# Kernel tuning notes

Measured on AMD Instinct MI355X. Metric: run time of the kernel, lower is better.

The kernel has to match this reference:

```python
import jax, jax.numpy as jnp
import numpy as np
from jax import lax

SCALES = (1, 4, 16, 64)
EPS = 1e-5
B, S, D, H, R, FF = 4, 1024, 512, 8, 4, 2048
C = D // len(SCALES)  # channels per temporal scale


def _ln(x, g, b):
    mu = jnp.mean(x, -1, keepdims=True)
    var = jnp.mean(jnp.square(x - mu), -1, keepdims=True)
    return (x - mu) * lax.rsqrt(var + EPS) * g + b


def _interp_linear(y, L_out):
    # y: [B, C, L_in]; torch F.interpolate(mode='linear', align_corners=False)
    L_in = y.shape[-1]
    if L_in == L_out:
        return y
    pos = (jnp.arange(L_out, dtype=jnp.float32) + 0.5) * (L_in / L_out) - 0.5
    pos = jnp.clip(pos, 0.0, L_in - 1)
    lo = jnp.floor(pos).astype(jnp.int32)
    hi = jnp.minimum(lo + 1, L_in - 1)
    w = (pos - lo.astype(jnp.float32))
    return y[..., lo] * (1.0 - w) + y[..., hi] * w


def _conv1d(x, w, b, stride):
    # x: [B, Cin, L], w: [Cout, Cin, K]
    y = lax.conv_general_dilated(x, w, window_strides=(stride,), padding='VALID',
                                 dimension_numbers=('NCH', 'OIH', 'NCH'))
    return y + b[None, :, None]


def setup_inputs() -> dict:
    key = jax.random.key(0)
    ks = jax.random.split(key, 40)
    n = lambda k, shp, s=0.02: jax.random.normal(k, shp, jnp.float32) * s
    inp = {}
    inp['x'] = jax.random.normal(ks[0], (B, S, D), jnp.float32)
    inp['resource_mask'] = jax.random.randint(ks[1], (B, S), 0, R, jnp.int32)
    inp['attention_mask'] = jnp.ones((B, S), jnp.int32)
    inp['wq'] = n(ks[2], (D, D)); inp['bq'] = jnp.zeros((D,), jnp.float32)
    inp['wk'] = n(ks[3], (D, D)); inp['bk'] = jnp.zeros((D,), jnp.float32)
    inp['wv'] = n(ks[4], (D, D)); inp['bv'] = jnp.zeros((D,), jnp.float32)
    inp['wo'] = n(ks[5], (D, D)); inp['bo'] = jnp.zeros((D,), jnp.float32)
    inp['rbias'] = jax.random.normal(ks[6], (H, R, R), jnp.float32)
    for i, sc in enumerate(SCALES):
        inp[f'cw{i}'] = n(ks[7 + i], (C, D, sc))
        inp[f'cb{i}'] = jnp.zeros((C,), jnp.float32)
    inp['fw'] = n(ks[12], (D, D)); inp['fb'] = jnp.zeros((D,), jnp.float32)
    inp['ltg'] = jnp.ones((D,), jnp.float32); inp['ltb'] = jnp.zeros((D,), jnp.float32)
    inp['n1g'] = jnp.ones((D,), jnp.float32); inp['n1b'] = jnp.zeros((D,), jnp.float32)
    inp['n2g'] = jnp.ones((D,), jnp.float32); inp['n2b'] = jnp.zeros((D,), jnp.float32)
    inp['fw1'] = n(ks[13], (FF, D)); inp['fb1'] = jnp.zeros((FF,), jnp.float32)
    inp['fw2'] = n(ks[14], (D, FF)); inp['fb2'] = jnp.zeros((D,), jnp.float32)
    inp['n3g'] = jnp.ones((D,), jnp.float32); inp['n3b'] = jnp.zeros((D,), jnp.float32)
    return inp


def reference(x, resource_mask, attention_mask, wq, bq, wk, bk, wv, bv, wo, bo, rbias,
              cw0, cb0, cw1, cb1, cw2, cb2, cw3, cb3, fw, fb, ltg, ltb,
              n1g, n1b, n2g, n2b, fw1, fb1, fw2, fb2, n3g, n3b):
    b_, s_, d_ = x.shape
    dk = d_ // H
    # --- ResourceAwareAttention (dropout = identity in eval) ---
    q = (x @ wq.T + bq).reshape(b_, s_, H, dk).transpose(0, 2, 1, 3)
    k = (x @ wk.T + bk).reshape(b_, s_, H, dk).transpose(0, 2, 1, 3)
    v = (x @ wv.T + bv).reshape(b_, s_, H, dk).transpose(0, 2, 1, 3)
    scores = jnp.einsum('bhid,bhjd->bhij', q, k) / jnp.sqrt(jnp.float32(dk))
    # vectorized resource-bias gather: bias[b,h,i,j] = rbias[h, rm[b,i], rm[b,j]]
    idx_h = jnp.arange(H)[None, :, None, None]
    idx_i = resource_mask[:, None, :, None]
    idx_j = resource_mask[:, None, None, :]
    scores = scores + rbias[idx_h, idx_i, idx_j]
    scores = jnp.where(attention_mask[:, None, None, :] == 0, -1e9, scores)
    attn = jax.nn.softmax(scores, axis=-1)
    o = jnp.einsum('bhij,bhjd->bhid', attn, v).transpose(0, 2, 1, 3).reshape(b_, s_, d_)
    attn_out = o @ wo.T + bo
    x = _ln(x + attn_out, n1g, n1b)
    # --- MultiScaleTemporalEncoder ---
    xc = x.transpose(0, 2, 1)  # [B, D, S]
    convs = ((cw0, cb0), (cw1, cb1), (cw2, cb2), (cw3, cb3))
    outs = []
    for sc, (w, bb) in zip(SCALES, convs):
        y = _conv1d(xc, w, bb, sc)  # [B, C, S/sc]
        outs.append(_interp_linear(y, s_))
    ms = jnp.concatenate(outs, axis=1).transpose(0, 2, 1)  # [B, S, D]
    fused = ms @ fw.T + fb
    temporal = _ln(x + fused, ltg, ltb)
    x = _ln(x + temporal, n2g, n2b)
    # --- FFN ---
    ff = jax.nn.relu(x @ fw1.T + fb1) @ fw2.T + fb2
    return _ln(x + ff, n3g, n3b)
```

## Files before the change

kernel.cpp:

```cpp
#include <hip/hip_runtime.h>
#include <math.h>

constexpr int B_ = 4, S_ = 1024, D_ = 512, H_ = 8, FF_ = 2048;
constexpr int DK_ = 64;
constexpr int C_ = 128;
constexpr int QKVLD = 1536;

typedef __bf16 bf16x8 __attribute__((ext_vector_type(8)));
typedef __bf16 bf16x4 __attribute__((ext_vector_type(4)));
typedef short short4v __attribute__((ext_vector_type(4)));
typedef float floatx4 __attribute__((ext_vector_type(4)));

__device__ __forceinline__ void g2l16(const __bf16* g, __bf16* l) {
  __builtin_amdgcn_global_load_lds(
      (__attribute__((address_space(1))) void*)(unsigned long long)g,
      (__attribute__((address_space(3))) void*)(unsigned int)(unsigned long long)l,
      16, 0, 0);
}

__device__ __forceinline__ int xcd_swz(int lin, int nwg) {
  return (lin & 7) * (nwg >> 3) + (lin >> 3);
}

template <bool OUTBF16, bool RELU, bool WRITEVT>
__global__ __launch_bounds__(256, 2) void mgemm(
    const __bf16* __restrict__ A, const __bf16* __restrict__ W,
    const float* __restrict__ bias, void* __restrict__ Yv,
    int M, int N, int K, int ldY, __bf16* __restrict__ VT) {
  __shared__ __bf16 As[2][128 * 64];
  __shared__ __bf16 Bs[2][128 * 64];
  const int tid = threadIdx.x;
  const int wave = tid >> 6, lane = tid & 63;
  const int nwg = gridDim.x * gridDim.y;
  const int lin = blockIdx.y * gridDim.x + blockIdx.x;
  const int swz = xcd_swz(lin, nwg);
  const int bm = (swz / gridDim.x) * 128, bn = (swz % gridDim.x) * 128;

  const int rsub = lane >> 3;
  const int gch = ((lane & 7) ^ rsub) * 8;
  const __bf16* gA = A + (size_t)(bm + wave * 32 + rsub) * K + gch;
  const __bf16* gB = W + (size_t)(bn + wave * 32 + rsub) * K + gch;

  const int mrow = lane & 15, g4 = lane >> 4;
  const int rsw = mrow & 7;
  const int wm = (wave & 1) * 64, wn = (wave >> 1) * 64;

  floatx4 acc[4][4];
#pragma unroll
  for (int mi = 0; mi < 4; mi++)
#pragma unroll
    for (int ni = 0; ni < 4; ni++) acc[mi][ni] = (floatx4){0.f, 0.f, 0.f, 0.f};

  const int nk = K >> 6;
  auto stage = [&](int buf, int kt) {
    const __bf16* ga = gA + (size_t)kt * 64;
    const __bf16* gb = gB + (size_t)kt * 64;
    __bf16* la = &As[buf][wave * 32 * 64];
    __bf16* lb = &Bs[buf][wave * 32 * 64];
#pragma unroll
    for (int i = 0; i < 4; i++) {
      g2l16(ga + (size_t)(i * 8) * K, la + i * 8 * 64);
      g2l16(gb + (size_t)(i * 8) * K, lb + i * 8 * 64);
    }
  };

  stage(0, 0);
  int cur = 0;
  for (int kk = 0; kk < nk; kk++) {
    __syncthreads();
    if (kk + 1 < nk) stage(cur ^ 1, kk + 1);
    const __bf16* Ab = As[cur];
    const __bf16* Bb = Bs[cur];
#pragma unroll
    for (int c = 0; c < 2; c++) {
      const int pc = (((c * 4 + g4) ^ rsw)) * 8;
      bf16x8 af[4], bfr[4];
#pragma unroll
      for (int mi = 0; mi < 4; mi++)
        af[mi] = *(const bf16x8*)(Ab + (wm + mi * 16 + mrow) * 64 + pc);
#pragma unroll
      for (int ni = 0; ni < 4; ni++)
        bfr[ni] = *(const bf16x8*)(Bb + (wn + ni * 16 + mrow) * 64 + pc);
#pragma unroll
      for (int mi = 0; mi < 4; mi++)
#pragma unroll
        for (int ni = 0; ni < 4; ni++)
          acc[mi][ni] = __builtin_amdgcn_mfma_f32_16x16x32_bf16(af[mi], bfr[ni], acc[mi][ni], 0, 0, 0);
    }
    cur ^= 1;
  }

  const int cc = lane & 15;
  const int r0 = (lane >> 4) * 4;
  float bv[4];
#pragma unroll
  for (int ni = 0; ni < 4; ni++) bv[ni] = bias[bn + wn + ni * 16 + cc];
#pragma unroll
  for (int mi = 0; mi < 4; mi++) {
#pragma unroll
    for (int ni = 0; ni < 4; ni++) {
      const int col = bn + wn + ni * 16 + cc;
      if (WRITEVT && col >= 1024) {
        const int h = (col - 1024) >> 6, d = (col - 1024) & 63;
        const int rowb = bm + wm + mi * 16 + r0;
        const int b = rowb >> 10, s = rowb & 1023;
        union { __bf16 hh[4]; unsigned long long u; } w;
#pragma unroll
        for (int i = 0; i < 4; i++) w.hh[i] = (__bf16)(acc[mi][ni][i] + bv[ni]);
        *(unsigned long long*)(VT + (size_t)(b * 8 + h) * 65536 + (size_t)d * 1024 + s) = w.u;
      } else {
#pragma unroll
        for (int i = 0; i < 4; i++) {
          float v = acc[mi][ni][i] + bv[ni];
          if (RELU) v = fmaxf(v, 0.f);
          const size_t row = bm + wm + mi * 16 + r0 + i;
          if (OUTBF16)
            ((__bf16*)Yv)[row * ldY + col] = (__bf16)v;
          else
            ((float*)Yv)[row * ldY + col] = v;
        }
      }
    }
  }
}

template <bool OUTBF16, bool RELU>
__global__ __launch_bounds__(256, 2) void mgemm64(
    const __bf16* __restrict__ A, const __bf16* __restrict__ W,
    const float* __restrict__ bias, void* __restrict__ Yv,
    int M, int N, int K, int ldY) {
  __shared__ __bf16 As[2][64 * 64];
  __shared__ __bf16 Bs[2][64 * 64];
  const int tid = threadIdx.x;
  const int wave = tid >> 6, lane = tid & 63;
  const int nwg = gridDim.x * gridDim.y;
  const int lin = blockIdx.y * gridDim.x + blockIdx.x;
  const int swz = xcd_swz(lin, nwg);
  const int bm = (swz / gridDim.x) * 64, bn = (swz % gridDim.x) * 64;

  const int rsub = lane >> 3;
  const int gch = ((lane & 7) ^ rsub) * 8;
  const __bf16* gA = A + (size_t)(bm + wave * 16 + rsub) * K + gch;
  const __bf16* gB = W + (size_t)(bn + wave * 16 + rsub) * K + gch;

  const int mrow = lane & 15, g4 = lane >> 4;
  const int rsw = mrow & 7;
  const int wm = (wave & 1) * 32, wn = (wave >> 1) * 32;

  floatx4 acc[2][2];
#pragma unroll
  for (int mi = 0; mi < 2; mi++)
#pragma unroll
    for (int ni = 0; ni < 2; ni++) acc[mi][ni] = (floatx4){0.f, 0.f, 0.f, 0.f};

  const int nk = K >> 6;
  auto stage = [&](int buf, int kt) {
    const __bf16* ga = gA + (size_t)kt * 64;
    const __bf16* gb = gB + (size_t)kt * 64;
    __bf16* la = &As[buf][wave * 16 * 64];
    __bf16* lb = &Bs[buf][wave * 16 * 64];
#pragma unroll
    for (int i = 0; i < 2; i++) {
      g2l16(ga + (size_t)(i * 8) * K, la + i * 8 * 64);
      g2l16(gb + (size_t)(i * 8) * K, lb + i * 8 * 64);
    }
  };

  stage(0, 0);
  int cur = 0;
  for (int kk = 0; kk < nk; kk++) {
    __syncthreads();
    if (kk + 1 < nk) stage(cur ^ 1, kk + 1);
    const __bf16* Ab = As[cur];
    const __bf16* Bb = Bs[cur];
#pragma unroll
    for (int c = 0; c < 2; c++) {
      const int pc = (((c * 4 + g4) ^ rsw)) * 8;
      bf16x8 af[2], bfr[2];
#pragma unroll
      for (int mi = 0; mi < 2; mi++)
        af[mi] = *(const bf16x8*)(Ab + (wm + mi * 16 + mrow) * 64 + pc);
#pragma unroll
      for (int ni = 0; ni < 2; ni++)
        bfr[ni] = *(const bf16x8*)(Bb + (wn + ni * 16 + mrow) * 64 + pc);
#pragma unroll
      for (int mi = 0; mi < 2; mi++)
#pragma unroll
        for (int ni = 0; ni < 2; ni++)
          acc[mi][ni] = __builtin_amdgcn_mfma_f32_16x16x32_bf16(af[mi], bfr[ni], acc[mi][ni], 0, 0, 0);
    }
    cur ^= 1;
  }

  const int cc = lane & 15;
  const int r0 = (lane >> 4) * 4;
  float bv[2];
#pragma unroll
  for (int ni = 0; ni < 2; ni++) bv[ni] = bias[bn + wn + ni * 16 + cc];
#pragma unroll
  for (int mi = 0; mi < 2; mi++) {
#pragma unroll
    for (int ni = 0; ni < 2; ni++) {
      const int col = bn + wn + ni * 16 + cc;
#pragma unroll
      for (int i = 0; i < 4; i++) {
        float v = acc[mi][ni][i] + bv[ni];
        if (RELU) v = fmaxf(v, 0.f);
        const size_t row = bm + wm + mi * 16 + r0 + i;
        if (OUTBF16)
          ((__bf16*)Yv)[row * ldY + col] = (__bf16)v;
        else
          ((float*)Yv)[row * ldY + col] = v;
      }
    }
  }
}

__global__ __launch_bounds__(256, 2) void cgemm3(
    const __bf16* __restrict__ A, const __bf16* __restrict__ w4,
    const __bf16* __restrict__ w16, const __bf16* __restrict__ w64,
    const __bf16* __restrict__ w1, const float* __restrict__ cb0,
    float* __restrict__ y1, float* __restrict__ y2, float* __restrict__ y3,
    __bf16* __restrict__ msb) {
  int id = blockIdx.x;
  const __bf16* W;
  float* yseg = nullptr;
  int M, K, bm, k0s;
  bool direct = false;
  if (id < 64) {
    W = w4; yseg = y1; M = 1024; K = 2048;
    bm = (id & 15) * 64; k0s = id >> 4;
  } else if (id < 128) {
    id -= 64;
    W = w16; yseg = y2; M = 256; K = 8192;
    bm = (id & 3) * 64; k0s = id >> 2;
  } else if (id < 192) {
    id -= 128;
    W = w64; yseg = y3; M = 64; K = 32768;
    bm = 0; k0s = id;
  } else {
    id -= 192;
    W = w1; M = 4096; K = 512;
    bm = id * 64; k0s = 0; direct = true;
  }
  const int k0 = k0s * 512;

  __shared__ __bf16 As[2][64 * 32];
  __shared__ __bf16 Bs[2][128 * 32];
  const int tid = threadIdx.x;
  const int wave = tid >> 6, lane = tid & 63;

  const int rs2 = lane >> 2;
  const int ssw2 = (rs2 & 3) ^ ((rs2 >> 2) & 3);
  const int gc2 = ((lane & 3) ^ ssw2) * 8;
  const __bf16* gA = A + (size_t)(bm + wave * 16 + rs2) * K + k0 + gc2;
  const __bf16* gB0 = W + (size_t)(wave * 16 + rs2) * K + k0 + gc2;
  const __bf16* gB1 = W + (size_t)(64 + wave * 16 + rs2) * K + k0 + gc2;

  const int mrow = lane & 15, g4 = lane >> 4;
  const int fsw = (lane & 3) ^ ((lane >> 2) & 3);
  const int fc = (g4 ^ fsw) & 3;

  floatx4 acc[8];
#pragma unroll
  for (int nj = 0; nj < 8; nj++) acc[nj] = (floatx4){0.f, 0.f, 0.f, 0.f};

  auto stage = [&](int buf, int kt) {
    const size_t ko = (size_t)kt * 32;
    g2l16(gA + ko, &As[buf][wave * 16 * 32]);
    g2l16(gB0 + ko, &Bs[buf][wave * 16 * 32]);
    g2l16(gB1 + ko, &Bs[buf][(64 + wave * 16) * 32]);
  };

  stage(0, 0);
  int cur = 0;
  for (int kk = 0; kk < 16; kk++) {
    __syncthreads();
    if (kk + 1 < 16) stage(cur ^ 1, kk + 1);
    bf16x8 af = *(const bf16x8*)(As[cur] + (wave * 16 + mrow) * 32 + fc * 8);
#pragma unroll
    for (int nj = 0; nj < 8; nj++) {
      bf16x8 bfv = *(const bf16x8*)(Bs[cur] + (nj * 16 + mrow) * 32 + fc * 8);
      acc[nj] = __builtin_amdgcn_mfma_f32_16x16x32_bf16(af, bfv, acc[nj], 0, 0, 0);
    }
    cur ^= 1;
  }

  const int cc = lane & 15;
  const int r0 = (lane >> 4) * 4;
  if (direct) {
#pragma unroll
    for (int nj = 0; nj < 8; nj++) {
      const float bb = cb0[nj * 16 + cc];
#pragma unroll
      for (int i = 0; i < 4; i++)
        msb[(size_t)(bm + wave * 16 + r0 + i) * 512 + nj * 16 + cc] =
            (__bf16)(acc[nj][i] + bb);
    }
  } else {
#pragma unroll
    for (int nj = 0; nj < 8; nj++)
#pragma unroll
      for (int i = 0; i < 4; i++)
        atomicAdd(&yseg[(size_t)(bm + wave * 16 + r0 + i) * 128 + nj * 16 + cc],
                  acc[nj][i]);
  }
}

__global__ __launch_bounds__(256) void prep(
    const float* __restrict__ cw1, const float* __restrict__ cw2,
    const float* __restrict__ cw3, __bf16* __restrict__ wt4,
    __bf16* __restrict__ wt16, __bf16* __restrict__ wt64,
    const float* __restrict__ s0, const float* __restrict__ s1,
    const float* __restrict__ s2, const float* __restrict__ s3,
    const float* __restrict__ s4, const float* __restrict__ s5,
    const float* __restrict__ s6, const float* __restrict__ s7,
    const float* __restrict__ s8,
    __bf16* __restrict__ d0, __bf16* __restrict__ d1, __bf16* __restrict__ d2,
    __bf16* __restrict__ d3, __bf16* __restrict__ d4, __bf16* __restrict__ d5,
    __bf16* __restrict__ d6, __bf16* __restrict__ d7, __bf16* __restrict__ d8,
    const float* __restrict__ bq, const float* __restrict__ bk,
    const float* __restrict__ bv, float* __restrict__ bqkv,
    const float* __restrict__ cb1, const float* __restrict__ cb2,
    const float* __restrict__ cb3, float* __restrict__ yall) {
  __shared__ float Ts[4608];
  const int tid = threadIdx.x;
  if (blockIdx.x < 1408) {
    int id = blockIdx.x;
    const float* cw;
    __bf16* wt;
    int lg, c, d0i, TD, L;
    if (id < 128) {
      cw = cw1; wt = wt4; lg = 2; c = id; d0i = 0; TD = 512; L = 2048;
    } else if (id < 384) {
      id -= 128;
      cw = cw2; wt = wt16; lg = 4; c = id >> 1; d0i = (id & 1) * 256; TD = 256; L = 4096;
    } else {
      id -= 384;
      cw = cw3; wt = wt64; lg = 6; c = id >> 3; d0i = (id & 7) * 64; TD = 64; L = 4096;
    }
    const int sc = 1 << lg;
    const int KD = 512 << lg;
    const float* src = cw + (size_t)c * KD + (size_t)d0i * sc;

    for (int f = tid * 4; f < L; f += 1024) {
      const float4 v = *(const float4*)(src + f);
      const float vv[4] = {v.x, v.y, v.z, v.w};
#pragma unroll
      for (int j = 0; j < 4; j++) {
        const int idx = f + j;
        const int dl = idx >> lg, k = idx & (sc - 1);
        Ts[dl * (sc + 1) + k] = vv[j];
      }
    }
    __syncthreads();

    for (int w = tid * 8; w < L; w += 2048) {
      const int kpos = w / TD;
      const int dl0 = w - kpos * TD;
      union { __bf16 hh[8]; bf16x8 v; } u;
#pragma unroll
      for (int j = 0; j < 8; j++)
        u.hh[j] = (__bf16)Ts[(dl0 + j) * (sc + 1) + kpos];
      *(bf16x8*)(wt + (size_t)c * KD + kpos * 512 + d0i + dl0) = u.v;
    }
    return;
  }

  const int qd = (blockIdx.x - 1408) * 256 + tid;
  if (qd < 384) {
    const int i = qd * 4;
    const float* s;
    int off;
    if (i < 512) { s = bq; off = 0; }
    else if (i < 1024) { s = bk; off = 512; }
    else { s = bv; off = 1024; }
    *(float4*)(bqkv + i) = *(const float4*)(s + i - off);
  }
  if (qd < 172032) {
    float bb;
    if (qd < 131072) bb = cb1[qd & 127];
    else if (qd < 163840) bb = cb2[qd & 127];
    else bb = cb3[qd & 127];
    yall[qd] = bb;
  }
  if (qd >= 1392640) return;
  const float* src;
  __bf16* dst;
  int base;
  if (qd < 524288) { src = s0; dst = d0; base = 0; }
  else if (qd < 589824) { src = s1; dst = d1; base = 524288; }
  else if (qd < 655360) { src = s2; dst = d2; base = 589824; }
  else if (qd < 720896) { src = s3; dst = d3; base = 655360; }
  else if (qd < 786432) { src = s4; dst = d4; base = 720896; }
  else if (qd < 851968) { src = s5; dst = d5; base = 786432; }
  else if (qd < 868352) { src = s6; dst = d6; base = 851968; }
  else if (qd < 1130496) { src = s7; dst = d7; base = 868352; }
  else { src = s8; dst = d8; base = 1130496; }
  const int local = qd - base;
  float4 v = *(const float4*)(src + (size_t)local * 4);
  union { __bf16 h[4]; unsigned long long u; } t;
  t.h[0] = (__bf16)v.x; t.h[1] = (__bf16)v.y;
  t.h[2] = (__bf16)v.z; t.h[3] = (__bf16)v.w;
  *(unsigned long long*)(dst + (size_t)local * 4) = t.u;
}

__global__ __launch_bounds__(256) void fattn(
    const __bf16* __restrict__ QKV, const __bf16* __restrict__ VT,
    const float* __restrict__ rbias, const int* __restrict__ rm,
    const int* __restrict__ amask, __bf16* __restrict__ O) {
  __shared__ __bf16 Ks[64 * 72];
  __shared__ __bf16 Vs[64 * 72];
  __shared__ float T[4 * 1032];

  const int tid = threadIdx.x, wave = tid >> 6, lane = tid & 63;
  const int nwg = gridDim.x * gridDim.y;
  const int lin = blockIdx.y * gridDim.x + blockIdx.x;
  const int swz = xcd_swz(lin, nwg);
  const int qb = swz % gridDim.x;
  const int bh = swz / gridDim.x;
  const int b = bh >> 3, h = bh & 7;
  const int q0 = qb * 64;
  const int cc = lane & 15, quad = lane >> 4;

  for (int j = tid; j < 1024; j += 256) {
    const int rv = rm[b * S_ + j];
    const float mk = amask[b * S_ + j] ? 1.f : 0.f;
#pragma unroll
    for (int ri = 0; ri < 4; ri++)
      T[ri * 1032 + j] = __expf(rbias[h * 16 + ri * 4 + rv]) * mk;
  }

  const int qrow = q0 + wave * 16;
  const int rmi = rm[b * S_ + qrow + cc];
  const float* Trow = T + rmi * 1032;

  const __bf16* Qr = QKV + (size_t)(b * S_ + qrow + cc) * QKVLD + h * 64;
  const bf16x8 qb0 = *(const bf16x8*)(Qr + quad * 8);
  const bf16x8 qb1 = *(const bf16x8*)(Qr + 32 + quad * 8);

  floatx4 of[4];
#pragma unroll
  for (int dc = 0; dc < 4; dc++) of[dc] = (floatx4){0.f, 0.f, 0.f, 0.f};
  float mold = -1e30f, l = 0.f;

  const __bf16* Kbase = QKV + (size_t)(b * S_) * QKVLD + 512 + h * 64;
  const __bf16* Vtbase = VT + (size_t)bh * 65536;
  const int srow = tid >> 2, sch = tid & 3;

  for (int jt = 0; jt < 16; jt++) {
    const int j0 = jt * 64;
    __syncthreads();
    {
      const __bf16* kg = Kbase + (size_t)(j0 + srow) * QKVLD;
      *(bf16x8*)(Ks + srow * 72 + sch * 8) = *(const bf16x8*)(kg + sch * 8);
      *(bf16x8*)(Ks + srow * 72 + 32 + sch * 8) = *(const bf16x8*)(kg + 32 + sch * 8);
      const __bf16* vg = Vtbase + (size_t)srow * 1024 + j0;
      *(bf16x8*)(Vs + srow * 72 + sch * 8) = *(const bf16x8*)(vg + sch * 8);
      *(bf16x8*)(Vs + srow * 72 + 32 + sch * 8) = *(const bf16x8*)(vg + 32 + sch * 8);
    }
    __syncthreads();

    floatx4 st[4];
    __builtin_amdgcn_s_setprio(1);
#pragma unroll
    for (int js = 0; js < 4; js++) {
      const bf16x8 ka0 = *(const bf16x8*)(Ks + (js * 16 + cc) * 72 + quad * 8);
      const bf16x8 ka1 = *(const bf16x8*)(Ks + (js * 16 + cc) * 72 + 32 + quad * 8);
      floatx4 s = (floatx4){0.f, 0.f, 0.f, 0.f};
      s = __builtin_amdgcn_mfma_f32_16x16x32_bf16(ka0, qb0, s, 0, 0, 0);
      s = __builtin_amdgcn_mfma_f32_16x16x32_bf16(ka1, qb1, s, 0, 0, 0);
      st[js] = s;
    }
    __builtin_amdgcn_s_setprio(0);

    float mxr = st[0][0];
#pragma unroll
    for (int js = 0; js < 4; js++)
#pragma unroll
      for (int i = 0; i < 4; i++) mxr = fmaxf(mxr, st[js][i]);
    mxr = fmaxf(mxr, __shfl_xor(mxr, 16));
    mxr = fmaxf(mxr, __shfl_xor(mxr, 32));
    const float mnew = fmaxf(mold, mxr * 0.125f);
    const float alpha = __expf(mold - mnew);
    mold = mnew;

    float rsum = 0.f;
    short4v pk[4];
#pragma unroll
    for (int js = 0; js < 4; js++) {
      const floatx4 Tv = *(const floatx4*)(Trow + j0 + js * 16 + quad * 4);
      union { __bf16 hh[4]; short4v s4; } u;
#pragma unroll
      for (int i = 0; i < 4; i++) {
        const float p = __expf(fmaf(st[js][i], 0.125f, -mnew)) * Tv[i];
        rsum += p;
        u.hh[i] = (__bf16)p;
      }
      pk[js] = u.s4;
    }
    rsum += __shfl_xor(rsum, 16);
    rsum += __shfl_xor(rsum, 32);
    l = l * alpha + rsum;

#pragma unroll
    for (int dc = 0; dc < 4; dc++)
#pragma unroll
      for (int i = 0; i < 4; i++) of[dc][i] *= alpha;

    __builtin_amdgcn_s_setprio(1);
#pragma unroll
    for (int dc = 0; dc < 4; dc++) {
#pragma unroll
      for (int js = 0; js < 4; js++) {
        union { bf16x4 v; short4v s4; } va;
        va.v = *(const bf16x4*)(Vs + (dc * 16 + cc) * 72 + js * 16 + quad * 4);
        of[dc] = __builtin_amdgcn_mfma_f32_16x16x16bf16_1k(va.s4, pk[js], of[dc], 0, 0, 0);
      }
    }
    __builtin_amdgcn_s_setprio(0);
  }

  const float invl = 1.f / l;
  __bf16* po = O + (size_t)(b * S_ + qrow + cc) * D_ + h * 64;
#pragma unroll
  for (int dc = 0; dc < 4; dc++) {
    union { __bf16 hh[4]; unsigned long long u; } w;
#pragma unroll
    for (int i = 0; i < 4; i++) w.hh[i] = (__bf16)(of[dc][i] * invl);
    *(unsigned long long*)(po + dc * 16 + quad * 4) = w.u;
  }
}

__global__ __launch_bounds__(256) void add_ln_kernel(
    const float* __restrict__ xa, const float* __restrict__ xb,
    const float* __restrict__ g, const float* __restrict__ be,
    float* __restrict__ out, __bf16* __restrict__ outb) {
  const int row = (blockIdx.x * 256 + threadIdx.x) >> 6;
  const int lane = threadIdx.x & 63;
  const float* pa = xa + (size_t)row * D_;
  const float* pb = xb + (size_t)row * D_;
  float v[8];
  float sum = 0.f;
#pragma unroll
  for (int i = 0; i < 8; i++) {
    int dd = lane + 64 * i;
    v[i] = pa[dd] + pb[dd];
    sum += v[i];
  }
#pragma unroll
  for (int off = 32; off; off >>= 1) sum += __shfl_xor(sum, off);
  const float mu = sum * (1.f / D_);
  float vs = 0.f;
#pragma unroll
  for (int i = 0; i < 8; i++) { float t = v[i] - mu; vs += t * t; }
#pragma unroll
  for (int off = 32; off; off >>= 1) vs += __shfl_xor(vs, off);
  const float inv = rsqrtf(vs * (1.f / D_) + 1e-5f);
  float* po = out + (size_t)row * D_;
#pragma unroll
  for (int i = 0; i < 8; i++) {
    int dd = lane + 64 * i;
    float o = (v[i] - mu) * inv * g[dd] + be[dd];
    po[dd] = o;
    if (outb) outb[(size_t)row * D_ + dd] = (__bf16)o;
  }
}

__global__ __launch_bounds__(256) void ln_chain_kernel(
    const float* __restrict__ x1, const float* __restrict__ fused,
    const float* __restrict__ ltg, const float* __restrict__ ltb,
    const float* __restrict__ n2g, const float* __restrict__ n2b,
    float* __restrict__ out, __bf16* __restrict__ outb) {
  const int row = (blockIdx.x * 256 + threadIdx.x) >> 6;
  const int lane = threadIdx.x & 63;
  const float* p1 = x1 + (size_t)row * D_;
  const float* pf = fused + (size_t)row * D_;
  float xv[8], u[8];
  float sum = 0.f;
#pragma unroll
  for (int i = 0; i < 8; i++) {
    int dd = lane + 64 * i;
    xv[i] = p1[dd];
    u[i] = xv[i] + pf[dd];
    sum += u[i];
  }
#pragma unroll
  for (int off = 32; off; off >>= 1) sum += __shfl_xor(sum, off);
  float mu = sum * (1.f / D_);
  float vs = 0.f;
#pragma unroll
  for (int i = 0; i < 8; i++) { float t = u[i] - mu; vs += t * t; }
#pragma unroll
  for (int off = 32; off; off >>= 1) vs += __shfl_xor(vs, off);
  float inv = rsqrtf(vs * (1.f / D_) + 1e-5f);
  float sum2 = 0.f;
#pragma unroll
  for (int i = 0; i < 8; i++) {
    int dd = lane + 64 * i;
    float t = (u[i] - mu) * inv * ltg[dd] + ltb[dd];
    u[i] = xv[i] + t;
    sum2 += u[i];
  }
#pragma unroll
  for (int off = 32; off; off >>= 1) sum2 += __shfl_xor(sum2, off);
  float mu2 = sum2 * (1.f / D_);
  float vs2 = 0.f;
#pragma unroll
  for (int i = 0; i < 8; i++) { float t = u[i] - mu2; vs2 += t * t; }
#pragma unroll
  for (int off = 32; off; off >>= 1) vs2 += __shfl_xor(vs2, off);
  float inv2 = rsqrtf(vs2 * (1.f / D_) + 1e-5f);
  float* po = out + (size_t)row * D_;
#pragma unroll
  for (int i = 0; i < 8; i++) {
    int dd = lane + 64 * i;
    float o = (u[i] - mu2) * inv2 * n2g[dd] + n2b[dd];
    po[dd] = o;
    outb[(size_t)row * D_ + dd] = (__bf16)o;
  }
}

__global__ void interp_kernel(const float* __restrict__ y1, const float* __restrict__ y2,
                              const float* __restrict__ y3, __bf16* __restrict__ ms) {
  int idx = blockIdx.x * 256 + threadIdx.x;
  if (idx >= B_ * S_ * 3 * C_) return;
  int c3 = idx % (3 * C_);
  int rest = idx / (3 * C_);
  int s = rest % S_, b = rest / S_;
  int i = c3 >> 7;
  int c = c3 & 127;
  int Lin = (i == 0) ? 256 : (i == 1) ? 64 : 16;
  const float* y = (i == 0) ? y1 : (i == 1) ? y2 : y3;
  float pos = (s + 0.5f) * ((float)Lin / S_) - 0.5f;
  pos = fminf(fmaxf(pos, 0.f), (float)(Lin - 1));
  int lo = (int)floorf(pos);
  int hi = min(lo + 1, Lin - 1);
  float w = pos - (float)lo;
  const float* ybase = y + ((size_t)(b * Lin + lo)) * 128 + c;
  float vlo = ybase[0];
  float vhi = ybase[(size_t)(hi - lo) * 128];
  ms[((size_t)b * S_ + s) * D_ + C_ + c3] = (__bf16)(vlo * (1.f - w) + vhi * w);
}

extern "C" void kernel_launch(void* const* d_in, const int* in_sizes, int n_in,
                              void* d_out, int out_size, void* d_ws, size_t ws_size,
                              hipStream_t stream) {
  const float* x   = (const float*)d_in[0];
  const int* rm    = (const int*)d_in[1];
  const int* am    = (const int*)d_in[2];
  const float* wq  = (const float*)d_in[3];
  const float* bq  = (const float*)d_in[4];
  const float* wk  = (const float*)d_in[5];
  const float* bk  = (const float*)d_in[6];
  const float* wv  = (const float*)d_in[7];
  const float* bv  = (const float*)d_in[8];
  const float* wo  = (const float*)d_in[9];
  const float* bo  = (const float*)d_in[10];
  const float* rbias = (const float*)d_in[11];
  const float* cw0 = (const float*)d_in[12];
  const float* cb0 = (const float*)d_in[13];
  const float* cw1 = (const float*)d_in[14];
  const float* cb1 = (const float*)d_in[15];
  const float* cw2 = (const float*)d_in[16];
  const float* cb2 = (const float*)d_in[17];
  const float* cw3 = (const float*)d_in[18];
  const float* cb3 = (const float*)d_in[19];
  const float* fw  = (const float*)d_in[20];
  const float* fb  = (const float*)d_in[21];
  const float* ltg = (const float*)d_in[22];
  const float* ltb = (const float*)d_in[23];
  const float* n1g = (const float*)d_in[24];
  const float* n1b = (const float*)d_in[25];
  const float* n2g = (const float*)d_in[26];
  const float* n2b = (const float*)d_in[27];
  const float* fw1 = (const float*)d_in[28];
  const float* fb1 = (const float*)d_in[29];
  const float* fw2 = (const float*)d_in[30];
  const float* fb2 = (const float*)d_in[31];
  const float* n3g = (const float*)d_in[32];
  const float* n3b = (const float*)d_in[33];

  float* ws = (float*)d_ws;
  __bf16* wqkvb = (__bf16*)(ws + 0);
  __bf16* wob   = (__bf16*)(ws + 393216);
  __bf16* fwb   = (__bf16*)(ws + 524288);
  __bf16* cw0b  = (__bf16*)(ws + 655360);
  __bf16* fw1b  = (__bf16*)(ws + 688128);
  __bf16* fw2b  = (__bf16*)(ws + 1212416);
  __bf16* xb    = (__bf16*)(ws + 1835008);
  __bf16* qkv   = (__bf16*)(ws + 2883584);
  __bf16* attnb = (__bf16*)(ws + 6029312);
  float*  x1    = ws + 7077888;
  __bf16* x1b   = (__bf16*)(ws + 9175040);
  float*  scr   = ws + 10223616;
  float*  x2    = ws + 12320768;
  __bf16* x2b   = (__bf16*)(ws + 14417920);
  __bf16* msb   = (__bf16*)(ws + 15466496);
  float*  y1    = ws + 16515072;
  float*  y2    = ws + 16646144;
  float*  y3    = ws + 16678912;
  float*  bqkv  = ws + 16687104;
  __bf16* wt4b  = (__bf16*)(ws + 16689152);
  __bf16* wt16b = (__bf16*)(ws + 16820224);
  __bf16* wt64b = (__bf16*)(ws + 17344512);
  __bf16* VT    = (__bf16*)(ws + 10223616);
  __bf16* ffh   = (__bf16*)(ws + 2883584);

  dim3 blk(256);

  prep<<<6848, blk, 0, stream>>>(
      cw1, cw2, cw3, wt4b, wt16b, wt64b,
      x, wq, wk, wv, wo, fw, cw0, fw1, fw2,
      xb, wqkvb, wqkvb + 262144, wqkvb + 524288, wob, fwb, cw0b, fw1b, fw2b,
      bq, bk, bv, bqkv, cb1, cb2, cb3, y1);

  mgemm<true, false, true><<<dim3(12, 32), blk, 0, stream>>>(
      xb, wqkvb, bqkv, qkv, 4096, 1536, 512, QKVLD, VT);

  fattn<<<dim3(16, 32), blk, 0, stream>>>(qkv, VT, rbias, rm, am, attnb);

  mgemm64<false, false><<<dim3(8, 64), blk, 0, stream>>>(
      attnb, wob, bo, scr, 4096, 512, 512, 512);
  add_ln_kernel<<<1024, blk, 0, stream>>>(x, scr, n1g, n1b, x1, x1b);

  cgemm3<<<256, blk, 0, stream>>>(x1b, wt4b, wt16b, wt64b, cw0b, cb0, y1, y2, y3, msb);
  interp_kernel<<<6144, blk, 0, stream>>>(y1, y2, y3, msb);

  mgemm64<false, false><<<dim3(8, 64), blk, 0, stream>>>(
      msb, fwb, fb, scr, 4096, 512, 512, 512);
  ln_chain_kernel<<<1024, blk, 0, stream>>>(x1, scr, ltg, ltb, n2g, n2b, x2, x2b);

  mgemm<true, true, false><<<dim3(16, 32), blk, 0, stream>>>(
      x2b, fw1b, fb1, ffh, 4096, 2048, 512, 2048, nullptr);
  mgemm64<false, false><<<dim3(8, 64), blk, 0, stream>>>(
      ffh, fw2b, fb2, scr, 4096, 512, 2048, 512);
  add_ln_kernel<<<1024, blk, 0, stream>>>(x2, scr, n3g, n3b, (float*)d_out, nullptr);
}
```

Measured before the change: 273.9 us.

## Double-buffer attention K/V loads, retile conv GEMM split-K, vectorize LN and interp

```diff
diff --git a/kernel.cpp b/kernel.cpp
--- a/kernel.cpp
+++ b/kernel.cpp
@@ -222,66 +222,67 @@
     const __bf16* __restrict__ w1, const float* __restrict__ cb0,
     float* __restrict__ y1, float* __restrict__ y2, float* __restrict__ y3,
     __bf16* __restrict__ msb) {
-  int id = blockIdx.x;
+  int id = xcd_swz(blockIdx.x, 448);
   const __bf16* W;
   float* yseg = nullptr;
-  int M, K, bm, k0s;
+  int K, bm, k0, nk;
   bool direct = false;
-  if (id < 64) {
-    W = w4; yseg = y1; M = 1024; K = 2048;
-    bm = (id & 15) * 64; k0s = id >> 4;
-  } else if (id < 128) {
-    id -= 64;
-    W = w16; yseg = y2; M = 256; K = 8192;
-    bm = (id & 3) * 64; k0s = id >> 2;
-  } else if (id < 192) {
+  if (id < 128) {
+    W = w4; yseg = y1; K = 2048; bm = (id & 15) * 64; k0 = (id >> 4) * 256; nk = 4;
+  } else if (id < 256) {
     id -= 128;
-    W = w64; yseg = y3; M = 64; K = 32768;
-    bm = 0; k0s = id;
+    W = w16; yseg = y2; K = 8192; bm = (id & 3) * 64; k0 = (id >> 2) * 256; nk = 4;
+  } else if (id < 384) {
+    id -= 256;
+    W = w64; yseg = y3; K = 32768; bm = 0; k0 = id * 256; nk = 4;
   } else {
-    id -= 192;
-    W = w1; M = 4096; K = 512;
-    bm = id * 64; k0s = 0; direct = true;
-  }
-  const int k0 = k0s * 512;
-
-  __shared__ __bf16 As[2][64 * 32];
-  __shared__ __bf16 Bs[2][128 * 32];
+    id -= 384;
+    W = w1; K = 512; bm = id * 64; k0 = 0; nk = 8; direct = true;
+  }
+
+  __shared__ __bf16 As[2][64 * 64];
+  __shared__ __bf16 Bs[2][128 * 64];
   const int tid = threadIdx.x;
   const int wave = tid >> 6, lane = tid & 63;
 
-  const int rs2 = lane >> 2;
-  const int ssw2 = (rs2 & 3) ^ ((rs2 >> 2) & 3);
-  const int gc2 = ((lane & 3) ^ ssw2) * 8;
-  const __bf16* gA = A + (size_t)(bm + wave * 16 + rs2) * K + k0 + gc2;
-  const __bf16* gB0 = W + (size_t)(wave * 16 + rs2) * K + k0 + gc2;
-  const __bf16* gB1 = W + (size_t)(64 + wave * 16 + rs2) * K + k0 + gc2;
+  const int rsub = lane >> 3;
+  const int gch = ((lane & 7) ^ rsub) * 8;
+  const __bf16* gA = A + (size_t)(bm + wave * 16 + rsub) * K + k0 + gch;
+  const __bf16* gB = W + (size_t)(wave * 32 + rsub) * K + k0 + gch;
 
   const int mrow = lane & 15, g4 = lane >> 4;
-  const int fsw = (lane & 3) ^ ((lane >> 2) & 3);
-  const int fc = (g4 ^ fsw) & 3;
+  const int rsw = mrow & 7;
 
   floatx4 acc[8];
 #pragma unroll
   for (int nj = 0; nj < 8; nj++) acc[nj] = (floatx4){0.f, 0.f, 0.f, 0.f};
 
   auto stage = [&](int buf, int kt) {
-    const size_t ko = (size_t)kt * 32;
-    g2l16(gA + ko, &As[buf][wave * 16 * 32]);
-    g2l16(gB0 + ko, &Bs[buf][wave * 16 * 32]);
-    g2l16(gB1 + ko, &Bs[buf][(64 + wave * 16) * 32]);
+    const size_t ko = (size_t)kt * 64;
+#pragma unroll
+    for (int i = 0; i < 2; i++)
+      g2l16(gA + ko + (size_t)(i * 8) * K, &As[buf][(wave * 16 + i * 8) * 64]);
+#pragma unroll
+    for (int i = 0; i < 4; i++)
+      g2l16(gB + ko + (size_t)(i * 8) * K, &Bs[buf][(wave * 32 + i * 8) * 64]);
   };
 
   stage(0, 0);
   int cur = 0;
-  for (int kk = 0; kk < 16; kk++) {
+  for (int kk = 0; kk < nk; kk++) {
     __syncthreads();
-    if (kk + 1 < 16) stage(cur ^ 1, kk + 1);
-    bf16x8 af = *(const bf16x8*)(As[cur] + (wave * 16 + mrow) * 32 + fc * 8);
-#pragma unroll
-    for (int nj = 0; nj < 8; nj++) {
-      bf16x8 bfv = *(const bf16x8*)(Bs[cur] + (nj * 16 + mrow) * 32 + fc * 8);
-      acc[nj] = __builtin_amdgcn_mfma_f32_16x16x32_bf16(af, bfv, acc[nj], 0, 0, 0);
+    if (kk + 1 < nk) stage(cur ^ 1, kk + 1);
+    const __bf16* Ab = As[cur];
+    const __bf16* Bb = Bs[cur];
+#pragma unroll
+    for (int c = 0; c < 2; c++) {
+      const int pc = (((c * 4 + g4) ^ rsw)) * 8;
+      bf16x8 af = *(const bf16x8*)(Ab + (wave * 16 + mrow) * 64 + pc);
+#pragma unroll
+      for (int nj = 0; nj < 8; nj++) {
+        bf16x8 bfv = *(const bf16x8*)(Bb + (nj * 16 + mrow) * 64 + pc);
+        acc[nj] = __builtin_amdgcn_mfma_f32_16x16x32_bf16(af, bfv, acc[nj], 0, 0, 0);
+      }
     }
     cur ^= 1;
   }
@@ -409,8 +410,8 @@
     const __bf16* __restrict__ QKV, const __bf16* __restrict__ VT,
     const float* __restrict__ rbias, const int* __restrict__ rm,
     const int* __restrict__ amask, __bf16* __restrict__ O) {
-  __shared__ __bf16 Ks[64 * 72];
-  __shared__ __bf16 Vs[64 * 72];
+  __shared__ __bf16 Ks[2][64 * 64];
+  __shared__ __bf16 Vs[2][64 * 64];
   __shared__ float T[4 * 1032];
 
   const int tid = threadIdx.x, wave = tid >> 6, lane = tid & 63;
@@ -444,29 +445,37 @@
   for (int dc = 0; dc < 4; dc++) of[dc] = (floatx4){0.f, 0.f, 0.f, 0.f};
   float mold = -1e30f, l = 0.f;
 
-  const __bf16* Kbase = QKV + (size_t)(b * S_) * QKVLD + 512 + h * 64;
-  const __bf16* Vtbase = VT + (size_t)bh * 65536;
-  const int srow = tid >> 2, sch = tid & 3;
+  const int rsub = lane >> 3;
+  const int sgch = ((lane & 7) ^ rsub) * 8;
+  const __bf16* Kg = QKV + (size_t)(b * S_ + wave * 16 + rsub) * QKVLD + 512 + h * 64 + sgch;
+  const __bf16* Vg = VT + (size_t)bh * 65536 + (size_t)(wave * 16 + rsub) * 1024 + sgch;
+
+  auto stage = [&](int buf, int jt) {
+    const int j0 = jt * 64;
+#pragma unroll
+    for (int i = 0; i < 2; i++) {
+      g2l16(Kg + (size_t)(j0 + i * 8) * QKVLD, &Ks[buf][(wave * 16 + i * 8) * 64]);
+      g2l16(Vg + j0 + (size_t)(i * 8) * 1024, &Vs[buf][(wave * 16 + i * 8) * 64]);
+    }
+  };
+
+  stage(0, 0);
+  int cur = 0;
+  const int rk = cc & 7;
 
   for (int jt = 0; jt < 16; jt++) {
     const int j0 = jt * 64;
     __syncthreads();
-    {
-      const __bf16* kg = Kbase + (size_t)(j0 + srow) * QKVLD;
-      *(bf16x8*)(Ks + srow * 72 + sch * 8) = *(const bf16x8*)(kg + sch * 8);
-      *(bf16x8*)(Ks + srow * 72 + 32 + sch * 8) = *(const bf16x8*)(kg + 32 + sch * 8);
-      const __bf16* vg = Vtbase + (size_t)srow * 1024 + j0;
-      *(bf16x8*)(Vs + srow * 72 + sch * 8) = *(const bf16x8*)(vg + sch * 8);
-      *(bf16x8*)(Vs + srow * 72 + 32 + sch * 8) = *(const bf16x8*)(vg + 32 + sch * 8);
-    }
-    __syncthreads();
+    if (jt + 1 < 16) stage(cur ^ 1, jt + 1);
+    const __bf16* Kb = Ks[cur];
+    const __bf16* Vb = Vs[cur];
 
     floatx4 st[4];
     __builtin_amdgcn_s_setprio(1);
 #pragma unroll
     for (int js = 0; js < 4; js++) {
-      const bf16x8 ka0 = *(const bf16x8*)(Ks + (js * 16 + cc) * 72 + quad * 8);
-      const bf16x8 ka1 = *(const bf16x8*)(Ks + (js * 16 + cc) * 72 + 32 + quad * 8);
+      const bf16x8 ka0 = *(const bf16x8*)(Kb + (js * 16 + cc) * 64 + ((quad ^ rk) * 8));
+      const bf16x8 ka1 = *(const bf16x8*)(Kb + (js * 16 + cc) * 64 + (((quad + 4) ^ rk) * 8));
       floatx4 s = (floatx4){0.f, 0.f, 0.f, 0.f};
       s = __builtin_amdgcn_mfma_f32_16x16x32_bf16(ka0, qb0, s, 0, 0, 0);
       s = __builtin_amdgcn_mfma_f32_16x16x32_bf16(ka1, qb1, s, 0, 0, 0);
@@ -514,11 +523,13 @@
 #pragma unroll
       for (int js = 0; js < 4; js++) {
         union { bf16x4 v; short4v s4; } va;
-        va.v = *(const bf16x4*)(Vs + (dc * 16 + cc) * 72 + js * 16 + quad * 4);
+        va.v = *(const bf16x4*)(Vb + (dc * 16 + cc) * 64 +
+                                (((js * 2 + (quad >> 1)) ^ rk) * 8) + (quad & 1) * 4);
         of[dc] = __builtin_amdgcn_mfma_f32_16x16x16bf16_1k(va.s4, pk[js], of[dc], 0, 0, 0);
       }
     }
     __builtin_amdgcn_s_setprio(0);
+    cur ^= 1;
   }
 
   const float invl = 1.f / l;
@@ -538,32 +549,41 @@
     float* __restrict__ out, __bf16* __restrict__ outb) {
   const int row = (blockIdx.x * 256 + threadIdx.x) >> 6;
   const int lane = threadIdx.x & 63;
-  const float* pa = xa + (size_t)row * D_;
-  const float* pb = xb + (size_t)row * D_;
-  float v[8];
+  const floatx4* pa = (const floatx4*)(xa + (size_t)row * D_);
+  const floatx4* pb = (const floatx4*)(xb + (size_t)row * D_);
+  floatx4 v[2];
   float sum = 0.f;
 #pragma unroll
-  for (int i = 0; i < 8; i++) {
-    int dd = lane + 64 * i;
+  for (int i = 0; i < 2; i++) {
+    const int dd = lane + 64 * i;
     v[i] = pa[dd] + pb[dd];
-    sum += v[i];
+    sum += v[i][0] + v[i][1] + v[i][2] + v[i][3];
   }
 #pragma unroll
   for (int off = 32; off; off >>= 1) sum += __shfl_xor(sum, off);
   const float mu = sum * (1.f / D_);
   float vs = 0.f;
 #pragma unroll
-  for (int i = 0; i < 8; i++) { float t = v[i] - mu; vs += t * t; }
+  for (int i = 0; i < 2; i++)
+#pragma unroll
+    for (int j = 0; j < 4; j++) { float t = v[i][j] - mu; vs += t * t; }
 #pragma unroll
   for (int off = 32; off; off >>= 1) vs += __shfl_xor(vs, off);
   const float inv = rsqrtf(vs * (1.f / D_) + 1e-5f);
-  float* po = out + (size_t)row * D_;
-#pragma unroll
-  for (int i = 0; i < 8; i++) {
-    int dd = lane + 64 * i;
-    float o = (v[i] - mu) * inv * g[dd] + be[dd];
+  floatx4* po = (floatx4*)(out + (size_t)row * D_);
+#pragma unroll
+  for (int i = 0; i < 2; i++) {
+    const int dd = lane + 64 * i;
+    const floatx4 g4 = ((const floatx4*)g)[dd];
+    const floatx4 b4 = ((const floatx4*)be)[dd];
+    const floatx4 o = (v[i] - mu) * inv * g4 + b4;
     po[dd] = o;
-    if (outb) outb[(size_t)row * D_ + dd] = (__bf16)o;
+    if (outb) {
+      union { __bf16 hh[4]; unsigned long long u; } w;
+#pragma unroll
+      for (int j = 0; j < 4; j++) w.hh[j] = (__bf16)o[j];
+      *(unsigned long long*)(outb + (size_t)row * D_ + dd * 4) = w.u;
+    }
   }
 }
 
@@ -574,73 +594,87 @@
     float* __restrict__ out, __bf16* __restrict__ outb) {
   const int row = (blockIdx.x * 256 + threadIdx.x) >> 6;
   const int lane = threadIdx.x & 63;
-  const float* p1 = x1 + (size_t)row * D_;
-  const float* pf = fused + (size_t)row * D_;
-  float xv[8], u[8];
+  const floatx4* p1 = (const floatx4*)(x1 + (size_t)row * D_);
+  const floatx4* pf = (const floatx4*)(fused + (size_t)row * D_);
+  floatx4 xv[2], u[2];
   float sum = 0.f;
 #pragma unroll
-  for (int i = 0; i < 8; i++) {
-    int dd = lane + 64 * i;
+  for (int i = 0; i < 2; i++) {
+    const int dd = lane + 64 * i;
     xv[i] = p1[dd];
     u[i] = xv[i] + pf[dd];
-    sum += u[i];
+    sum += u[i][0] + u[i][1] + u[i][2] + u[i][3];
   }
 #pragma unroll
   for (int off = 32; off; off >>= 1) sum += __shfl_xor(sum, off);
   float mu = sum * (1.f / D_);
   float vs = 0.f;
 #pragma unroll
-  for (int i = 0; i < 8; i++) { float t = u[i] - mu; vs += t * t; }
+  for (int i = 0; i < 2; i++)
+#pragma unroll
+    for (int j = 0; j < 4; j++) { float t = u[i][j] - mu; vs += t * t; }
 #pragma unroll
   for (int off = 32; off; off >>= 1) vs += __shfl_xor(vs, off);
   float inv = rsqrtf(vs * (1.f / D_) + 1e-5f);
   float sum2 = 0.f;
 #pragma unroll
-  for (int i = 0; i < 8; i++) {
-    int dd = lane + 64 * i;
-    float t = (u[i] - mu) * inv * ltg[dd] + ltb[dd];
-    u[i] = xv[i] + t;
-    sum2 += u[i];
+  for (int i = 0; i < 2; i++) {
+    const int dd = lane + 64 * i;
+    const floatx4 g4 = ((const floatx4*)ltg)[dd];
+    const floatx4 b4 = ((const floatx4*)ltb)[dd];
+    u[i] = xv[i] + ((u[i] - mu) * inv * g4 + b4);
+    sum2 += u[i][0] + u[i][1] + u[i][2] + u[i][3];
   }
 #pragma unroll
   for (int off = 32; off; off >>= 1) sum2 += __shfl_xor(sum2, off);
   float mu2 = sum2 * (1.f / D_);
   float vs2 = 0.f;
 #pragma unroll
-  for (int i = 0; i < 8; i++) { float t = u[i] - mu2; vs2 += t * t; }
+  for (int i = 0; i < 2; i++)
+#pragma unroll
+    for (int j = 0; j < 4; j++) { float t = u[i][j] - mu2; vs2 += t * t; }
 #pragma unroll
   for (int off = 32; off; off >>= 1) vs2 += __shfl_xor(vs2, off);
   float inv2 = rsqrtf(vs2 * (1.f / D_) + 1e-5f);
-  float* po = out + (size_t)row * D_;
-#pragma unroll
-  for (int i = 0; i < 8; i++) {
-    int dd = lane + 64 * i;
-    float o = (u[i] - mu2) * inv2 * n2g[dd] + n2b[dd];
+  floatx4* po = (floatx4*)(out + (size_t)row * D_);
+#pragma unroll
+  for (int i = 0; i < 2; i++) {
+    const int dd = lane + 64 * i;
+    const floatx4 g4 = ((const floatx4*)n2g)[dd];
+    const floatx4 b4 = ((const floatx4*)n2b)[dd];
+    const floatx4 o = (u[i] - mu2) * inv2 * g4 + b4;
     po[dd] = o;
-    outb[(size_t)row * D_ + dd] = (__bf16)o;
+    union { __bf16 hh[4]; unsigned long long u8; } w;
+#pragma unroll
+    for (int j = 0; j < 4; j++) w.hh[j] = (__bf16)o[j];
+    *(unsigned long long*)(outb + (size_t)row * D_ + dd * 4) = w.u8;
   }
 }
 
 __global__ void interp_kernel(const float* __restrict__ y1, const float* __restrict__ y2,
                               const float* __restrict__ y3, __bf16* __restrict__ ms) {
   int idx = blockIdx.x * 256 + threadIdx.x;
-  if (idx >= B_ * S_ * 3 * C_) return;
-  int c3 = idx % (3 * C_);
-  int rest = idx / (3 * C_);
-  int s = rest % S_, b = rest / S_;
-  int i = c3 >> 7;
-  int c = c3 & 127;
-  int Lin = (i == 0) ? 256 : (i == 1) ? 64 : 16;
+  if (idx >= B_ * S_ * 3 * C_ / 4) return;
+  const int c3_4 = idx % 96;
+  const int rest = idx / 96;
+  const int s = rest & 1023, b = rest >> 10;
+  const int i = c3_4 >> 5;
+  const int c = (c3_4 & 31) * 4;
+  const int Lin = (i == 0) ? 256 : (i == 1) ? 64 : 16;
   const float* y = (i == 0) ? y1 : (i == 1) ? y2 : y3;
   float pos = (s + 0.5f) * ((float)Lin / S_) - 0.5f;
   pos = fminf(fmaxf(pos, 0.f), (float)(Lin - 1));
-  int lo = (int)floorf(pos);
-  int hi = min(lo + 1, Lin - 1);
-  float w = pos - (float)lo;
+  const int lo = (int)floorf(pos);
+  const int hi = min(lo + 1, Lin - 1);
+  const float w = pos - (float)lo;
   const float* ybase = y + ((size_t)(b * Lin + lo)) * 128 + c;
-  float vlo = ybase[0];
-  float vhi = ybase[(size_t)(hi - lo) * 128];
-  ms[((size_t)b * S_ + s) * D_ + C_ + c3] = (__bf16)(vlo * (1.f - w) + vhi * w);
+  const floatx4 vlo = *(const floatx4*)ybase;
+  const floatx4 vhi = *(const floatx4*)(ybase + (size_t)(hi - lo) * 128);
+  const floatx4 o = vlo * (1.f - w) + vhi * w;
+  union { __bf16 hh[4]; unsigned long long u; } t;
+#pragma unroll
+  for (int j = 0; j < 4; j++) t.hh[j] = (__bf16)o[j];
+  *(unsigned long long*)(ms + ((size_t)b * S_ + s) * D_ + C_ + i * 128 + c) = t.u;
 }
 
 extern "C" void kernel_launch(void* const* d_in, const int* in_sizes, int n_in,
@@ -724,8 +758,8 @@
       attnb, wob, bo, scr, 4096, 512, 512, 512);
   add_ln_kernel<<<1024, blk, 0, stream>>>(x, scr, n1g, n1b, x1, x1b);
 
-  cgemm3<<<256, blk, 0, stream>>>(x1b, wt4b, wt16b, wt64b, cw0b, cb0, y1, y2, y3, msb);
-  interp_kernel<<<6144, blk, 0, stream>>>(y1, y2, y3, msb);
+  cgemm3<<<448, blk, 0, stream>>>(x1b, wt4b, wt16b, wt64b, cw0b, cb0, y1, y2, y3, msb);
+  interp_kernel<<<1536, blk, 0, stream>>>(y1, y2, y3, msb);
 
   mgemm64<false, false><<<dim3(8, 64), blk, 0, stream>>>(
       msb, fwb, fb, scr, 4096, 512, 512, 512);
```

New measurement: 271.3 us. No clear change (-0.9%).
